# Kernel tuning notes

Hardware: AMD Instinct MI355X
Metric: run time of the kernel (lower is better)

## Reference

```python
import jax, jax.numpy as jnp
import numpy as np
from math import sqrt

N = 50000
E = 800000
D_EMB = 512
DK = 64
DV = 64
HEADS = 8


def setup_inputs() -> dict:
    key = jax.random.key(0)
    k1, k2, k3, k4 = jax.random.split(key, 4)
    x = jax.random.normal(k1, (N, D_EMB), dtype=jnp.float32)
    edge_index = jax.random.randint(k2, (2, E), 0, N, dtype=jnp.int64)
    out_qkv = (2 * DK + DV) * HEADS  # 1536
    W_qkv = jax.random.normal(k3, (out_qkv, D_EMB), dtype=jnp.float32) / sqrt(D_EMB)
    b_qkv = jnp.zeros((out_qkv,), dtype=jnp.float32)
    W_ff = jax.random.normal(k4, (D_EMB, DV * HEADS), dtype=jnp.float32) / sqrt(DV * HEADS)
    b_ff = jnp.zeros((D_EMB,), dtype=jnp.float32)
    return {"x": x, "edge_index": edge_index, "W_qkv": W_qkv, "b_qkv": b_qkv,
            "W_ff": W_ff, "b_ff": b_ff}


def _attention_message(Q, K, V, senders, receivers, n_nodes):
    # Q,K: [N, H, dK], V: [N, H, dV]; edge lists: [E]
    scale = 1.0 / sqrt(Q.shape[-1])
    # per-edge scores: [E, H]
    scores = jnp.einsum('ehd,ehd->eh', Q[receivers], K[senders]) * scale
    # segment softmax over incoming edges of each receiver
    smax = jax.ops.segment_max(scores, receivers, num_segments=n_nodes)  # [N, H]
    ex = jnp.exp(scores - smax[receivers])                               # [E, H]
    denom = jax.ops.segment_sum(ex, receivers, num_segments=n_nodes)    # [N, H]
    att = ex / denom[receivers]                                         # [E, H]
    # weighted scatter of V from senders to receivers: [N, H, dV]
    out = jax.ops.segment_sum(att[:, :, None] * V[senders], receivers,
                              num_segments=n_nodes)
    return out, att


def reference(x, edge_index, W_qkv, b_qkv, W_ff, b_ff):
    n_nodes = x.shape[0]
    qkv = x @ W_qkv.T + b_qkv  # [N, (2*dK+dV)*H]
    Q, K, V = jnp.split(qkv, [DK * HEADS, 2 * DK * HEADS], axis=-1)
    Q = Q.reshape(n_nodes, HEADS, DK)
    K = K.reshape(n_nodes, HEADS, DK)
    V = V.reshape(n_nodes, HEADS, DV)
    senders, receivers = edge_index[0], edge_index[1]
    msg, _ = _attention_message(Q, K, V, senders, receivers, n_nodes)
    # aggregate_heads: flatten heads and project to d_Embedding
    out = msg.reshape(n_nodes, HEADS * DV) @ W_ff.T + b_ff
    return out
```

## Files before the change

kernel.cpp:

```cpp
#include <hip/hip_runtime.h>

static constexpr int NN = 50000;
static constexpr int NE = 800000;
static constexpr int DEMB = 512;
static constexpr int QKV_OUT = 1536;

typedef _Float16 half8 __attribute__((ext_vector_type(8)));
typedef float floatx4 __attribute__((ext_vector_type(4)));

#define KQ_SCALE (127.0f / 5.5f)
#define KQ_DEQ   (5.5f / 127.0f)

static constexpr size_t OFF_QH   = 0;
static constexpr size_t OFF_K8   = 51200000;
static constexpr size_t OFF_V8   = 76800000;
static constexpr size_t OFF_MSG  = 102400000;
static constexpr size_t OFF_SRT  = 153600000;
static constexpr size_t OFF_DEG  = 156800000;
static constexpr size_t OFF_OFFA = 157000000;
static constexpr size_t OFF_CUR  = 157200064;
static constexpr size_t OFF_FLAG = 157400064;
static constexpr size_t OFF_WQH  = 157400128;
static constexpr size_t OFF_WFH  = 158972992;

typedef __attribute__((address_space(1))) const void* gas_ptr;
typedef __attribute__((address_space(3))) void* lds_ptr_t;

__device__ __forceinline__ void load_lds16(const void* g, void* l) {
  __builtin_amdgcn_global_load_lds((gas_ptr)g, (lds_ptr_t)l, 16, 0, 0);
}

__global__ __launch_bounds__(256)
void k_cvt(const float* __restrict__ in, _Float16* __restrict__ out, int n8) {
  int i = blockIdx.x * 256 + threadIdx.x;
  if (i < n8) {
    floatx4 a = *(const floatx4*)(in + (size_t)i * 8);
    floatx4 b = *(const floatx4*)(in + (size_t)i * 8 + 4);
    half8 h;
    #pragma unroll
    for (int q = 0; q < 4; ++q) { h[q] = (_Float16)a[q]; h[q + 4] = (_Float16)b[q]; }
    *(half8*)(out + (size_t)i * 8) = h;
  }
}

__global__ __launch_bounds__(64)
void k_detect64(const void* __restrict__ edge, int* __restrict__ flag) {
  if (threadIdx.x == 0) {
    const int* p = (const int*)edge;
    int is64 = 1;
    for (int i = 0; i < 16; ++i) if (p[2 * i + 1] != 0) is64 = 0;
    *flag = is64;
  }
}

__device__ __forceinline__ int edge_at(const void* edge, int row, int e, int is64) {
  if (is64) return (int)((const long long*)edge)[(size_t)row * NE + e];
  return ((const int*)edge)[(size_t)row * NE + e];
}

__global__ __launch_bounds__(256)
void k_histo(const void* __restrict__ edge, const int* __restrict__ flag,
             int* __restrict__ deg) {
  int e = blockIdx.x * 256 + threadIdx.x;
  if (e < NE) {
    int r = edge_at(edge, 1, e, *flag);
    atomicAdd(&deg[r], 1);
  }
}

__global__ __launch_bounds__(1024)
void k_scan(const int* __restrict__ deg, int* __restrict__ off,
            int* __restrict__ cur, int n) {
  __shared__ int sums[1024];
  int tid = threadIdx.x;
  int per = (n + 1023) >> 10;
  int start = tid * per;
  int end = start + per; if (end > n) end = n;
  int s = 0;
  for (int i = start; i < end; ++i) s += deg[i];
  sums[tid] = s;
  __syncthreads();
  for (int d = 1; d < 1024; d <<= 1) {
    int v = (tid >= d) ? sums[tid - d] : 0;
    __syncthreads();
    sums[tid] += v;
    __syncthreads();
  }
  int run = (tid == 0) ? 0 : sums[tid - 1];
  for (int i = start; i < end; ++i) {
    off[i] = run; cur[i] = run; run += deg[i];
  }
  if (tid == 0) off[n] = sums[1023];
}

__global__ __launch_bounds__(256)
void k_scatter(const void* __restrict__ edge, const int* __restrict__ flag,
               int* __restrict__ cur, int* __restrict__ srt) {
  int e = blockIdx.x * 256 + threadIdx.x;
  if (e < NE) {
    int is64 = *flag;
    int r = edge_at(edge, 1, e, is64);
    int s = edge_at(edge, 0, e, is64);
    int pos = atomicAdd(&cur[r], 1);
    srt[pos] = s;
  }
}

template<int MODE>
__global__ __launch_bounds__(512, 2)
void k_gemm256(const _Float16* __restrict__ Ah, const _Float16* __restrict__ Bh,
               const float* __restrict__ bias,
               void* __restrict__ out0, void* __restrict__ out1, void* __restrict__ out2,
               int M, int N, int K, int nxt) {
  __shared__ _Float16 lds[2][2][2][256 * 32];
  const int tid = threadIdx.x;

  const int nwg = gridDim.x;
  const int cpx = nwg >> 3;
  const int w = (blockIdx.x & 7) * cpx + (blockIdx.x >> 3);
  const int m0 = (w / nxt) * 256;
  const int n0 = (w % nxt) * 256;

  const int wid = tid >> 6, lane = tid & 63;
  const int wr = wid >> 2, wc = wid & 3;

  floatx4 acc[8][4];
  #pragma unroll
  for (int m = 0; m < 8; ++m)
    #pragma unroll
    for (int n = 0; n < 4; ++n)
      #pragma unroll
      for (int q = 0; q < 4; ++q) acc[m][n][q] = 0.f;

  const int srow = tid >> 2;
  const int schunk = (tid & 3) ^ ((tid >> 3) & 3);
  int garow[2];
  #pragma unroll
  for (int c = 0; c < 2; ++c) {
    int gr = m0 + c * 128 + srow;
    garow[c] = gr < M ? gr : M - 1;
  }
  const int gbrow0 = n0 + srow, gbrow1 = n0 + 128 + srow;

  const int fr = lane & 15;
  const int fs = lane >> 4;

  const int KT = K >> 6;

  auto STAGE = [&](int tt, int kk) {
    const size_t kbase = (size_t)tt * 64 + kk * 32 + schunk * 8;
    char* La = (char*)&lds[tt & 1][kk][0][0];
    char* Lb = (char*)&lds[tt & 1][kk][1][0];
    load_lds16(Ah + (size_t)garow[0] * K + kbase, La + tid * 16);
    load_lds16(Ah + (size_t)garow[1] * K + kbase, La + 8192 + tid * 16);
    load_lds16(Bh + (size_t)gbrow0 * K + kbase, Lb + tid * 16);
    load_lds16(Bh + (size_t)gbrow1 * K + kbase, Lb + 8192 + tid * 16);
  };

  STAGE(0, 0);
  STAGE(0, 1);
  __syncthreads();

  for (int t = 0; t < KT; ++t) {
    const bool st = (t + 1 < KT);
    #pragma unroll
    for (int kk = 0; kk < 2; ++kk) {
      if (st) STAGE(t + 1, kk);
      const _Float16* La = &lds[t & 1][kk][0][0];
      const _Float16* Lb = &lds[t & 1][kk][1][0];
      half8 a[8], b[4];
      #pragma unroll
      for (int m = 0; m < 8; ++m) {
        int R = wr * 128 + m * 16 + fr;
        int s = fs ^ ((R >> 1) & 3);
        a[m] = *(const half8*)(La + R * 32 + s * 8);
      }
      #pragma unroll
      for (int n = 0; n < 4; ++n) {
        int R = wc * 64 + n * 16 + fr;
        int s = fs ^ ((R >> 1) & 3);
        b[n] = *(const half8*)(Lb + R * 32 + s * 8);
      }
      __builtin_amdgcn_s_setprio(1);
      #pragma unroll
      for (int m = 0; m < 8; ++m)
        #pragma unroll
        for (int n = 0; n < 4; ++n)
          acc[m][n] = __builtin_amdgcn_mfma_f32_16x16x32_f16(a[m], b[n], acc[m][n], 0, 0, 0);
      __builtin_amdgcn_s_setprio(0);
      if (st) asm volatile("s_waitcnt vmcnt(4)" ::: "memory");
      else    asm volatile("s_waitcnt vmcnt(0)" ::: "memory");
      __builtin_amdgcn_s_barrier();
    }
  }

  const int fq = fs << 2;
  #pragma unroll
  for (int m = 0; m < 8; ++m) {
    #pragma unroll
    for (int n = 0; n < 4; ++n) {
      int gn = n0 + wc * 64 + n * 16 + fr;
      float bv = bias[gn];
      #pragma unroll
      for (int q = 0; q < 4; ++q) {
        int gm = m0 + wr * 128 + m * 16 + fq + q;
        if (gm < M) {
          float val = acc[m][n][q] + bv;
          if (MODE == 0) {
            int region = gn >> 9;
            int col = gn & 511;
            size_t idx = (size_t)gm * 512 + col;
            if (region == 0) ((_Float16*)out0)[idx] = (_Float16)val;
            else {
              float s = fminf(fmaxf(val * KQ_SCALE, -127.f), 127.f);
              signed char c = (signed char)__float2int_rn(s);
              if (region == 1) ((signed char*)out1)[idx] = c;
              else             ((signed char*)out2)[idx] = c;
            }
          } else {
            ((float*)out0)[(size_t)gm * N + gn] = val;
          }
        }
      }
    }
  }
}

__global__ __launch_bounds__(256)
void k_attn(const _Float16* __restrict__ Qh, const signed char* __restrict__ K8,
            const signed char* __restrict__ V8, const int* __restrict__ off,
            const int* __restrict__ srt, _Float16* __restrict__ msg) {
  int r = blockIdx.x * 4 + (threadIdx.x >> 6);
  if (r >= NN) return;
  int lane = threadIdx.x & 63;
  int h = lane >> 3, j = lane & 7;
  int qoff = h * 64 + j * 8;

  half8 qh = *(const half8*)(Qh + (size_t)r * 512 + qoff);
  float q[8];
  #pragma unroll
  for (int i = 0; i < 8; ++i) q[i] = (float)qh[i] * 0.125f * KQ_DEQ;

  float denom = 0.f;
  float acc[8];
  #pragma unroll
  for (int i = 0; i < 8; ++i) acc[i] = 0.f;

  int e0 = off[r], e1 = off[r + 1];
  if (e1 <= e0) {
    half8 z = {};
    *(half8*)(msg + (size_t)r * 512 + qoff) = z;
    return;
  }

  auto gload = [&](uint2& k8, uint2& v8, int s) {
    k8 = *(const uint2*)(K8 + (size_t)s * 512 + qoff);
    v8 = *(const uint2*)(V8 + (size_t)s * 512 + qoff);
  };
  auto consume = [&](uint2 k8, uint2 v8) {
    int xw = (int)k8.x, yw = (int)k8.y;
    float p = 0.f;
    p += q[0] * (float)((xw << 24) >> 24);
    p += q[1] * (float)((xw << 16) >> 24);
    p += q[2] * (float)((xw << 8) >> 24);
    p += q[3] * (float)(xw >> 24);
    p += q[4] * (float)((yw << 24) >> 24);
    p += q[5] * (float)((yw << 16) >> 24);
    p += q[6] * (float)((yw << 8) >> 24);
    p += q[7] * (float)(yw >> 24);
    p += __shfl_xor(p, 1);
    p += __shfl_xor(p, 2);
    p += __shfl_xor(p, 4);
    float w = __expf(p);
    denom += w;
    int vx = (int)v8.x, vy = (int)v8.y;
    acc[0] += w * (float)((vx << 24) >> 24);
    acc[1] += w * (float)((vx << 16) >> 24);
    acc[2] += w * (float)((vx << 8) >> 24);
    acc[3] += w * (float)(vx >> 24);
    acc[4] += w * (float)((vy << 24) >> 24);
    acc[5] += w * (float)((vy << 16) >> 24);
    acc[6] += w * (float)((vy << 8) >> 24);
    acc[7] += w * (float)(vy >> 24);
  };
  auto sidx = [&](int e) { return srt[e < e1 ? e : e1 - 1]; };

  uint2 kb0, kb1, kb2, kb3, vb0, vb1, vb2, vb3;
  gload(kb0, vb0, sidx(e0));
  gload(kb1, vb1, sidx(e0 + 1));
  gload(kb2, vb2, sidx(e0 + 2));
  gload(kb3, vb3, sidx(e0 + 3));
  int sn0 = sidx(e0 + 4), sn1 = sidx(e0 + 5), sn2 = sidx(e0 + 6), sn3 = sidx(e0 + 7);

  int e = e0;
  for (; e + 4 <= e1; e += 4) {
    consume(kb0, vb0); gload(kb0, vb0, sn0);
    consume(kb1, vb1); gload(kb1, vb1, sn1);
    consume(kb2, vb2); gload(kb2, vb2, sn2);
    consume(kb3, vb3); gload(kb3, vb3, sn3);
    sn0 = sidx(e + 8); sn1 = sidx(e + 9); sn2 = sidx(e + 10); sn3 = sidx(e + 11);
  }
  int rem = e1 - e;
  if (rem > 0) consume(kb0, vb0);
  if (rem > 1) consume(kb1, vb1);
  if (rem > 2) consume(kb2, vb2);

  float inv = KQ_DEQ / denom;
  half8 oh;
  #pragma unroll
  for (int i = 0; i < 8; ++i) oh[i] = (_Float16)(acc[i] * inv);
  *(half8*)(msg + (size_t)r * 512 + qoff) = oh;
}

extern "C" void kernel_launch(void* const* d_in, const int* in_sizes, int n_in,
                              void* d_out, int out_size, void* d_ws, size_t ws_size,
                              hipStream_t stream) {
  const float* x     = (const float*)d_in[0];
  const void*  edge  = d_in[1];
  const float* W_qkv = (const float*)d_in[2];
  const float* b_qkv = (const float*)d_in[3];
  const float* W_ff  = (const float*)d_in[4];
  const float* b_ff  = (const float*)d_in[5];
  float* out = (float*)d_out;

  char* ws = (char*)d_ws;
  _Float16* Qh = (_Float16*)(ws + OFF_QH);
  signed char* K8 = (signed char*)(ws + OFF_K8);
  signed char* V8 = (signed char*)(ws + OFF_V8);
  _Float16* msgb = (_Float16*)(ws + OFF_MSG);
  _Float16* xh   = (_Float16*)(ws + OFF_MSG);
  int* srt  = (int*)(ws + OFF_SRT);
  int* deg  = (int*)(ws + OFF_DEG);
  int* offa = (int*)(ws + OFF_OFFA);
  int* cur  = (int*)(ws + OFF_CUR);
  int* flag = (int*)(ws + OFF_FLAG);
  _Float16* wqh = (_Float16*)(ws + OFF_WQH);
  _Float16* wfh = (_Float16*)(ws + OFF_WFH);

  hipMemsetAsync(deg, 0, NN * sizeof(int), stream);
  k_detect64<<<1, 64, 0, stream>>>(edge, flag);

  k_cvt<<<(NN * DEMB / 8 + 255) / 256, 256, 0, stream>>>(x, xh, NN * DEMB / 8);
  k_cvt<<<(QKV_OUT * DEMB / 8 + 255) / 256, 256, 0, stream>>>(W_qkv, wqh, QKV_OUT * DEMB / 8);
  k_cvt<<<(DEMB * DEMB / 8 + 255) / 256, 256, 0, stream>>>(W_ff, wfh, DEMB * DEMB / 8);

  k_gemm256<0><<<1176, 512, 0, stream>>>(
      xh, wqh, b_qkv, Qh, K8, V8, NN, QKV_OUT, DEMB, 6);

  k_histo<<<(NE + 255) / 256, 256, 0, stream>>>(edge, flag, deg);
  k_scan<<<1, 1024, 0, stream>>>(deg, offa, cur, NN);
  k_scatter<<<(NE + 255) / 256, 256, 0, stream>>>(edge, flag, cur, srt);

  k_attn<<<(NN + 3) / 4, 256, 0, stream>>>(Qh, K8, V8, offa, srt, msgb);

  k_gemm256<1><<<392, 512, 0, stream>>>(
      msgb, wfh, b_ff, out, nullptr, nullptr, NN, DEMB, DEMB, 2);
}
```

Before: 605.8 us.

## Switch GEMM LDS staging to triple-buffered 32-wide K slices

```diff
diff --git a/kernel.cpp b/kernel.cpp
--- a/kernel.cpp
+++ b/kernel.cpp
@@ -112,7 +112,7 @@
                const float* __restrict__ bias,
                void* __restrict__ out0, void* __restrict__ out1, void* __restrict__ out2,
                int M, int N, int K, int nxt) {
-  __shared__ _Float16 lds[2][2][2][256 * 32];
+  __shared__ _Float16 lds[3][2][256 * 32];
   const int tid = threadIdx.x;
 
   const int nwg = gridDim.x;
@@ -133,65 +133,57 @@
       for (int q = 0; q < 4; ++q) acc[m][n][q] = 0.f;
 
   const int srow = tid >> 2;
-  const int schunk = (tid & 3) ^ ((tid >> 3) & 3);
-  int garow[2];
-  #pragma unroll
-  for (int c = 0; c < 2; ++c) {
-    int gr = m0 + c * 128 + srow;
-    garow[c] = gr < M ? gr : M - 1;
-  }
+  const int schunk = (tid & 3) ^ ((srow >> 1) & 3);
+  int garow0 = m0 + srow;        if (garow0 >= M) garow0 = M - 1;
+  int garow1 = m0 + 128 + srow;  if (garow1 >= M) garow1 = M - 1;
   const int gbrow0 = n0 + srow, gbrow1 = n0 + 128 + srow;
 
   const int fr = lane & 15;
   const int fs = lane >> 4;
 
-  const int KT = K >> 6;
-
-  auto STAGE = [&](int tt, int kk) {
-    const size_t kbase = (size_t)tt * 64 + kk * 32 + schunk * 8;
-    char* La = (char*)&lds[tt & 1][kk][0][0];
-    char* Lb = (char*)&lds[tt & 1][kk][1][0];
-    load_lds16(Ah + (size_t)garow[0] * K + kbase, La + tid * 16);
-    load_lds16(Ah + (size_t)garow[1] * K + kbase, La + 8192 + tid * 16);
-    load_lds16(Bh + (size_t)gbrow0 * K + kbase, Lb + tid * 16);
-    load_lds16(Bh + (size_t)gbrow1 * K + kbase, Lb + 8192 + tid * 16);
+  const int KT = K >> 5;
+
+  auto STAGE = [&](int tt) {
+    const size_t kb = (size_t)(tt << 5) + schunk * 8;
+    char* La = (char*)&lds[tt % 3][0][0];
+    char* Lb = (char*)&lds[tt % 3][1][0];
+    load_lds16(Ah + (size_t)garow0 * K + kb, La + tid * 16);
+    load_lds16(Ah + (size_t)garow1 * K + kb, La + 8192 + tid * 16);
+    load_lds16(Bh + (size_t)gbrow0 * K + kb, Lb + tid * 16);
+    load_lds16(Bh + (size_t)gbrow1 * K + kb, Lb + 8192 + tid * 16);
   };
 
-  STAGE(0, 0);
-  STAGE(0, 1);
-  __syncthreads();
+  STAGE(0);
+  STAGE(1);
+  asm volatile("s_waitcnt vmcnt(4)" ::: "memory");
+  __builtin_amdgcn_s_barrier();
 
   for (int t = 0; t < KT; ++t) {
-    const bool st = (t + 1 < KT);
-    #pragma unroll
-    for (int kk = 0; kk < 2; ++kk) {
-      if (st) STAGE(t + 1, kk);
-      const _Float16* La = &lds[t & 1][kk][0][0];
-      const _Float16* Lb = &lds[t & 1][kk][1][0];
-      half8 a[8], b[4];
+    const bool st = (t + 2 < KT);
+    if (st) STAGE(t + 2);
+    const _Float16* La = &lds[t % 3][0][0];
+    const _Float16* Lb = &lds[t % 3][1][0];
+    half8 a[8], b[4];
+    #pragma unroll
+    for (int m = 0; m < 8; ++m) {
+      int R = wr * 128 + m * 16 + fr;
+      int s = fs ^ ((R >> 1) & 3);
+      a[m] = *(const half8*)(La + R * 32 + s * 8);
+    }
+    #pragma unroll
+    for (int n = 0; n < 4; ++n) {
+      int R = wc * 64 + n * 16 + fr;
+      int s = fs ^ ((R >> 1) & 3);
+      b[n] = *(const half8*)(Lb + R * 32 + s * 8);
+    }
+    #pragma unroll
+    for (int m = 0; m < 8; ++m)
       #pragma unroll
-      for (int m = 0; m < 8; ++m) {
-        int R = wr * 128 + m * 16 + fr;
-        int s = fs ^ ((R >> 1) & 3);
-        a[m] = *(const half8*)(La + R * 32 + s * 8);
-      }
-      #pragma unroll
-      for (int n = 0; n < 4; ++n) {
-        int R = wc * 64 + n * 16 + fr;
-        int s = fs ^ ((R >> 1) & 3);
-        b[n] = *(const half8*)(Lb + R * 32 + s * 8);
-      }
-      __builtin_amdgcn_s_setprio(1);
-      #pragma unroll
-      for (int m = 0; m < 8; ++m)
-        #pragma unroll
-        for (int n = 0; n < 4; ++n)
-          acc[m][n] = __builtin_amdgcn_mfma_f32_16x16x32_f16(a[m], b[n], acc[m][n], 0, 0, 0);
-      __builtin_amdgcn_s_setprio(0);
-      if (st) asm volatile("s_waitcnt vmcnt(4)" ::: "memory");
-      else    asm volatile("s_waitcnt vmcnt(0)" ::: "memory");
-      __builtin_amdgcn_s_barrier();
-    }
+      for (int n = 0; n < 4; ++n)
+        acc[m][n] = __builtin_amdgcn_mfma_f32_16x16x32_f16(a[m], b[n], acc[m][n], 0, 0, 0);
+    if (st) asm volatile("s_waitcnt vmcnt(4)" ::: "memory");
+    else    asm volatile("s_waitcnt vmcnt(0)" ::: "memory");
+    __builtin_amdgcn_s_barrier();
   }
 
   const int fq = fs << 2;
```

Result: no change. 606.8 us (+0.2%).
